# Kernel optimization log

Measured on AMD Instinct MI355X. Metric: run time of the kernel, lower is better.

## Reference

```python
import jax, jax.numpy as jnp
import numpy as np
from jax import lax

B, N, D, H, HD = 2, 2048, 2048, 16, 128
EPS = 1e-6


def setup_inputs() -> dict:
    key = jax.random.key(0)
    ks = jax.random.split(key, 6)
    x = jax.random.normal(ks[0], (B, N, D), jnp.float32)
    past_kv = jnp.zeros((B, H, HD, HD), jnp.float32)
    # positive per-head decay slopes, like MiniMax's ALiBi-style slope_rate
    slope_rate = jax.random.uniform(ks[1], (H, 1, 1), jnp.float32, 0.001, 0.1)
    w_qkv = jax.random.normal(ks[2], (3 * H * HD, D), jnp.float32) * 0.02
    w_gate = jax.random.normal(ks[3], (H * HD, D), jnp.float32) * 0.02
    w_out = jax.random.normal(ks[4], (D, H * HD), jnp.float32) * 0.02
    norm_w = jnp.ones((H * HD,), jnp.float32)
    return {"x": x, "past_kv": past_kv, "slope_rate": slope_rate,
            "w_qkv": w_qkv, "w_gate": w_gate, "w_out": w_out, "norm_w": norm_w}


def reference(x, past_kv, slope_rate, w_qkv, w_gate, w_out, norm_w):
    b, n, d = x.shape
    h = slope_rate.shape[0]
    hd = past_kv.shape[-1]

    # qkv projection + silu activation
    qkv = jax.nn.silu(x @ w_qkv.T)                 # [b, n, 3*h*hd]
    qkv = qkv.reshape(b, n, h, 3 * hd)
    q, k, v = jnp.split(qkv, 3, axis=-1)           # each [b, n, h, hd]
    # time-major for scan: [n, b, h, hd]
    q = jnp.transpose(q, (1, 0, 2, 3))
    k = jnp.transpose(k, (1, 0, 2, 3))
    v = jnp.transpose(v, (1, 0, 2, 3))

    ratio = jnp.exp(-slope_rate)                   # [h, 1, 1] broadcasts vs kv [b, h, hd, hd]

    def step(kv, qkv_t):
        q_t, k_t, v_t = qkv_t                      # each [b, h, hd]
        kv = ratio * kv + k_t[..., :, None] * v_t[..., None, :]   # [b, h, dk, dv]
        o = jnp.einsum('bhe,bhed->bhd', q_t, kv)   # contract over k-dim
        return kv, o

    kv_final, out = lax.scan(step, past_kv, (q, k, v))   # out: [n, b, h, hd]
    out = jnp.transpose(out, (1, 0, 2, 3)).reshape(b, n, h * hd)

    # RMSNorm over h*hd (computed in fp32 as in the original)
    var = jnp.mean(out * out, axis=-1, keepdims=True)
    out = norm_w * (out * lax.rsqrt(var + EPS))

    # sigmoid output gate + final projection
    gate = jax.nn.sigmoid(x @ w_gate.T)            # [b, n, h*hd]
    out = (gate * out) @ w_out.T                   # [b, n, d]
    return out, kv_final
```

## Files before the change

kernel.cpp:

```cpp
#include <hip/hip_runtime.h>


typedef __attribute__((ext_vector_type(8))) short short8;
typedef __attribute__((ext_vector_type(4))) float f32x4;

__device__ __forceinline__ float blo(unsigned int u){ return __uint_as_float(u << 16); }
__device__ __forceinline__ float bhi(unsigned int u){ return __uint_as_float(u & 0xffff0000u); }
__device__ __forceinline__ unsigned short f2b(float f){
  unsigned int u = __float_as_uint(f);
  return (unsigned short)((u + 0x7fffu + ((u >> 16) & 1u)) >> 16);
}
__device__ __forceinline__ unsigned int pk2(float a, float b){
  return (unsigned int)f2b(a) | ((unsigned int)f2b(b) << 16);
}

#define GLOAD_LDS16(g, l) __builtin_amdgcn_global_load_lds( \
    (const __attribute__((address_space(1))) unsigned int*)(g), \
    (__attribute__((address_space(3))) unsigned int*)(l), 16, 0, 0)

#define FRAG(buf, row, kt) (*(const short8*)&(buf)[(((row) << 7)) + \
    ((((((kt) << 2) + lk)) ^ ((row) & 15)) << 3)])

#define OFF_XB     ((size_t)0)
#define OFF_WQKVB  ((size_t)16777216)
#define OFF_WGATEB ((size_t)41943040)
#define OFF_WOUTB  ((size_t)50331648)
#define OFF_QB     ((size_t)58720256)
#define OFF_KB     ((size_t)75497472)
#define OFF_VTB    ((size_t)92274688)
#define OFF_KVC    ((size_t)109051904)
#define OFF_ATTN   ((size_t)142606336)
#define OFF_GATE   ((size_t)176160768)
#define OFF_YBUF   ((size_t)192937984)
#define WS_NEED    ((size_t)209715200)

__global__ __launch_bounds__(256)
void cast_f2b(const float* __restrict__ in, unsigned short* __restrict__ o, int n)
{
  int idx = (blockIdx.x * 256 + threadIdx.x) * 4;
  if (idx >= n) return;
  float4 v = *(const float4*)&in[idx];
  ushort4 u;
  u.x = f2b(v.x); u.y = f2b(v.y); u.z = f2b(v.z); u.w = f2b(v.w);
  *(ushort4*)&o[idx] = u;
}

template<int EPI>
__global__ __launch_bounds__(256)
void gemm_bt(const unsigned short* __restrict__ A, const unsigned short* __restrict__ Bm,
             int K, int Nn, void* __restrict__ o0, void* __restrict__ o1,
             void* __restrict__ o2, void* __restrict__ o3,
             const float* __restrict__ slope)
{
  __shared__ unsigned short As[4096];
  __shared__ unsigned short Bs[4096];
  const int tid  = threadIdx.x;
  const int lane = tid & 63, w = tid >> 6;
  const int mBase = blockIdx.y << 7, nBase = blockIdx.x << 7;

  f32x4 zero = {0.f, 0.f, 0.f, 0.f};
  f32x4 acc[4][4];
#pragma unroll
  for (int m = 0; m < 4; ++m)
#pragma unroll
    for (int n = 0; n < 4; ++n) acc[m][n] = zero;

  const int wr = w >> 1, wc = w & 1;
  const int rA = (wr << 6) + (lane & 15);
  const int cB = (wc << 6) + (lane & 15);
  const int kg = (lane >> 4) << 3;
  const int segBase = w << 7;
  const int nIter = K >> 5;

  for (int kt = 0; kt < nIter; ++kt) {
    const int k0 = kt << 5;
#pragma unroll
    for (int rep = 0; rep < 2; ++rep) {
      int seg = segBase + (rep << 6) + lane;
      int r  = seg >> 2;
      int c8 = (seg & 3) << 3;
      GLOAD_LDS16(A  + ((size_t)(mBase + r) * K + k0 + c8), &As[(segBase + (rep << 6)) << 3]);
      GLOAD_LDS16(Bm + ((size_t)(nBase + r) * K + k0 + c8), &Bs[(segBase + (rep << 6)) << 3]);
    }
    __syncthreads();
    short8 af[4], bfv[4];
#pragma unroll
    for (int m = 0; m < 4; ++m) af[m]  = *(const short8*)&As[((rA + (m << 4)) << 5) + kg];
#pragma unroll
    for (int n = 0; n < 4; ++n) bfv[n] = *(const short8*)&Bs[((cB + (n << 4)) << 5) + kg];
#pragma unroll
    for (int m = 0; m < 4; ++m)
#pragma unroll
      for (int n = 0; n < 4; ++n)
        acc[m][n] = __builtin_amdgcn_mfma_f32_16x16x32_bf16(af[m], bfv[n], acc[m][n], 0, 0, 0);
    __syncthreads();
  }

#pragma unroll
  for (int m = 0; m < 4; ++m) {
#pragma unroll
    for (int n = 0; n < 4; ++n) {
      const int row0 = mBase + (wr << 6) + (m << 4) + ((lane >> 4) << 2);
      const int col  = nBase + (wc << 6) + (n << 4) + (lane & 15);
      f32x4 v = acc[m][n];
#pragma unroll
      for (int i2 = 0; i2 < 4; ++i2) {
        const int row = row0 + i2;
        float val = v[i2];
        if (EPI == 0) {
          ((float*)o0)[(size_t)row * Nn + col] = val;
        } else if (EPI == 1) {
          float sv = val / (1.f + __expf(-val));
          int hh = col / 384;
          int r3 = col - hh * 384;
          int which = r3 >> 7;
          int dd = r3 & 127;
          int bb = row >> 11, nn = row & 2047;
          int bh = bb * 16 + hh;
          unsigned short sb = f2b(sv);
          size_t toff = ((size_t)bh << 18) + ((size_t)(nn >> 7) << 14)
                      + ((size_t)dd << 7) + (size_t)(nn & 127);
          if (which == 0) {
            ((unsigned short*)o0)[(((size_t)bh << 11) + nn) * 128 + dd] = sb;
          } else if (which == 1) {
            ((unsigned short*)o1)[(((size_t)bh << 11) + nn) * 128 + dd] = sb;
            float lam = __expf(-slope[hh] * (float)(127 - (nn & 127)));
            ((unsigned short*)o3)[toff] = f2b(sv * lam);
          } else {
            ((unsigned short*)o2)[toff] = sb;
          }
        } else {
          float sg = 1.f / (1.f + __expf(-val));
          ((unsigned short*)o0)[(size_t)row * Nn + col] = f2b(sg);
        }
      }
    }
  }
}

__global__ __launch_bounds__(256, 2)
void chunk_kv_mfma(const unsigned short* __restrict__ vtg,
                   const unsigned short* __restrict__ ktg,
                   float* __restrict__ KVc)
{
  __shared__ unsigned short VTs[16384], KTs[16384];
  const int blk = blockIdx.x;
  const int tid = threadIdx.x, lane = tid & 63, w = tid >> 6;
  const int wr = w >> 1, wc = w & 1, lr = lane & 15, lk = lane >> 4;
  const size_t base = (size_t)blk << 14;
#pragma unroll
  for (int it = 0; it < 8; ++it) {
    int segw = (w << 3) + it;
    int sg = (segw << 6) + lane;
    int r = sg >> 4, sl = sg & 15;
    size_t goff = ((size_t)r << 7) + (size_t)((sl ^ (r & 15)) << 3);
    GLOAD_LDS16(vtg + base + goff, &VTs[segw << 9]);
    GLOAD_LDS16(ktg + base + goff, &KTs[segw << 9]);
  }
  __syncthreads();
  f32x4 zero = {0.f,0.f,0.f,0.f};
  f32x4 acc[4][4];
#pragma unroll
  for (int m = 0; m < 4; ++m)
#pragma unroll
    for (int n = 0; n < 4; ++n) acc[m][n] = zero;
#pragma unroll
  for (int kt = 0; kt < 4; ++kt) {
    short8 af[4], bf2[4];
#pragma unroll
    for (int m = 0; m < 4; ++m) af[m]  = FRAG(VTs, (wr << 6) + (m << 4) + lr, kt);
#pragma unroll
    for (int n = 0; n < 4; ++n) bf2[n] = FRAG(KTs, (wc << 6) + (n << 4) + lr, kt);
#pragma unroll
    for (int m = 0; m < 4; ++m)
#pragma unroll
      for (int n = 0; n < 4; ++n)
        acc[m][n] = __builtin_amdgcn_mfma_f32_16x16x32_bf16(af[m], bf2[n], acc[m][n], 0, 0, 0);
  }
  float* outp = KVc + base;
#pragma unroll
  for (int m = 0; m < 4; ++m)
#pragma unroll
    for (int n = 0; n < 4; ++n)
#pragma unroll
      for (int r2 = 0; r2 < 4; ++r2)
        outp[(size_t)((wr << 6) + (m << 4) + (lk << 2) + r2) * 128
             + (wc << 6) + (n << 4) + lr] = acc[m][n][r2];
}

__global__ __launch_bounds__(256)
void combine_kv(float* __restrict__ KVc, const float* __restrict__ past_kv,
                const float* __restrict__ slope, float* __restrict__ outkv)
{
  const int bh = blockIdx.x >> 3, slice = blockIdx.x & 7;
  const int h = bh & 15;
  const int tid = threadIdx.x;
  const float lamC = __expf(-slope[h] * 128.f);
  const int f0 = (slice << 11) + tid;
  float S[8];
  const float* pp = past_kv + ((size_t)bh << 14);
#pragma unroll
  for (int i = 0; i < 8; ++i) {
    int f = f0 + (i << 8);
    int d = f >> 7, e = f & 127;
    S[i] = pp[(e << 7) + d];
  }
  for (int cc = 0; cc < 16; ++cc) {
    float* p = KVc + ((((size_t)bh << 4) + cc) << 14);
#pragma unroll
    for (int i = 0; i < 8; ++i) {
      int f = f0 + (i << 8);
      float t = p[f];
      p[f] = S[i];
      S[i] = lamC * S[i] + t;
    }
  }
  float* op = outkv + ((size_t)bh << 14);
#pragma unroll
  for (int i = 0; i < 8; ++i) {
    int f = f0 + (i << 8);
    int d = f >> 7, e = f & 127;
    op[(e << 7) + d] = S[i];
  }
}

__global__ __launch_bounds__(256, 1)
void chunk_out_mfma(const unsigned short* __restrict__ qg,
                    const unsigned short* __restrict__ kg,
                    const unsigned short* __restrict__ vtg,
                    const float* __restrict__ States,
                    const float* __restrict__ slope,
                    float* __restrict__ attn)
{
  __shared__ unsigned short Qs[16384], Ks[16384], VTs[16384], STs[16384];
  const int blk = blockIdx.x;
  const int cc = blk & 15, h = (blk >> 4) & 15, b = blk >> 8;
  const int tid = threadIdx.x, lane = tid & 63, w = tid >> 6;
  const int wr = w >> 1, wc = w & 1, lr = lane & 15, lk = lane >> 4;
  const size_t base = (size_t)blk << 14;
  const float s = slope[h];

#pragma unroll
  for (int it = 0; it < 8; ++it) {
    int segw = (w << 3) + it;
    int sg = (segw << 6) + lane;
    int r = sg >> 4, sl = sg & 15;
    size_t goff = ((size_t)r << 7) + (size_t)((sl ^ (r & 15)) << 3);
    GLOAD_LDS16(qg  + base + goff, &Qs[segw << 9]);
    GLOAD_LDS16(kg  + base + goff, &Ks[segw << 9]);
    GLOAD_LDS16(vtg + base + goff, &VTs[segw << 9]);
  }
  const float* Sg = States + base;
#pragma unroll
  for (int it = 0; it < 8; ++it) {
    int idx = ((it << 8) + tid) << 3;
    float4 a0 = *(const float4*)&Sg[idx];
    float4 a1 = *(const float4*)&Sg[idx + 4];
    int r = idx >> 7, c = idx & 127;
    int sl = (c >> 3) ^ (r & 15);
    uint4 u = make_uint4(pk2(a0.x,a0.y), pk2(a0.z,a0.w), pk2(a1.x,a1.y), pk2(a1.z,a1.w));
    *(uint4*)&STs[(r << 7) + (sl << 3)] = u;
  }
  __syncthreads();

  f32x4 zero = {0.f,0.f,0.f,0.f};
  f32x4 Oa[4][4], Pa[4][4];
#pragma unroll
  for (int m = 0; m < 4; ++m)
#pragma unroll
    for (int n = 0; n < 4; ++n) { Oa[m][n] = zero; Pa[m][n] = zero; }

#pragma unroll
  for (int kt = 0; kt < 4; ++kt) {
    short8 qf[4], bst[4], bk[4];
#pragma unroll
    for (int m = 0; m < 4; ++m) qf[m] = FRAG(Qs, (wr << 6) + (m << 4) + lr, kt);
#pragma unroll
    for (int n = 0; n < 4; ++n) {
      int cn = (wc << 6) + (n << 4) + lr;
      bst[n] = FRAG(STs, cn, kt);
      bk[n]  = FRAG(Ks,  cn, kt);
    }
#pragma unroll
    for (int m = 0; m < 4; ++m)
#pragma unroll
      for (int n = 0; n < 4; ++n) {
        Oa[m][n] = __builtin_amdgcn_mfma_f32_16x16x32_bf16(qf[m], bst[n], Oa[m][n], 0, 0, 0);
        Pa[m][n] = __builtin_amdgcn_mfma_f32_16x16x32_bf16(qf[m], bk[n],  Pa[m][n], 0, 0, 0);
      }
  }

  float emi[16];
#pragma unroll
  for (int m = 0; m < 4; ++m)
#pragma unroll
    for (int r2 = 0; r2 < 4; ++r2)
      emi[(m << 2) + r2] = __expf(-s * (float)((wr << 6) + (m << 4) + (lk << 2) + r2));
  const float lam1 = __expf(-s);
  float epj[4];
#pragma unroll
  for (int n = 0; n < 4; ++n)
    epj[n] = __expf(s * (float)((wc << 6) + (n << 4) + lr));

#pragma unroll
  for (int m = 0; m < 4; ++m)
#pragma unroll
    for (int n = 0; n < 4; ++n) {
      const int j = (wc << 6) + (n << 4) + lr;
#pragma unroll
      for (int r2 = 0; r2 < 4; ++r2) {
        const int i = (wr << 6) + (m << 4) + (lk << 2) + r2;
        Oa[m][n][r2] *= emi[(m << 2) + r2] * lam1;
        float pv = Pa[m][n][r2] * emi[(m << 2) + r2] * epj[n];
        Pa[m][n][r2] = (i >= j) ? pv : 0.f;
      }
    }
  __syncthreads();

#pragma unroll
  for (int m = 0; m < 4; ++m)
#pragma unroll
    for (int n = 0; n < 4; ++n) {
      const int j = (wc << 6) + (n << 4) + lr;
#pragma unroll
      for (int r2 = 0; r2 < 4; ++r2) {
        const int i = (wr << 6) + (m << 4) + (lk << 2) + r2;
        const int sl = (j >> 3) ^ (i & 15);
        Ks[(i << 7) + (sl << 3) + (j & 7)] = f2b(Pa[m][n][r2]);
      }
    }
  __syncthreads();

#pragma unroll
  for (int kt = 0; kt < 4; ++kt) {
    short8 pf[4], vf[4];
#pragma unroll
    for (int m = 0; m < 4; ++m) pf[m] = FRAG(Ks,  (wr << 6) + (m << 4) + lr, kt);
#pragma unroll
    for (int n = 0; n < 4; ++n) vf[n] = FRAG(VTs, (wc << 6) + (n << 4) + lr, kt);
#pragma unroll
    for (int m = 0; m < 4; ++m)
#pragma unroll
      for (int n = 0; n < 4; ++n)
        Oa[m][n] = __builtin_amdgcn_mfma_f32_16x16x32_bf16(pf[m], vf[n], Oa[m][n], 0, 0, 0);
  }

#pragma unroll
  for (int m = 0; m < 4; ++m)
#pragma unroll
    for (int n = 0; n < 4; ++n) {
      const int c = (wc << 6) + (n << 4) + lr;
#pragma unroll
      for (int r2 = 0; r2 < 4; ++r2) {
        const int i = (wr << 6) + (m << 4) + (lk << 2) + r2;
        attn[(((size_t)((b << 11) + (cc << 7) + i)) << 11) + (h << 7) + c] = Oa[m][n][r2];
      }
    }
}

__global__ __launch_bounds__(256)
void norm_gate(const float* __restrict__ attn, const unsigned short* __restrict__ gateb,
               const float* __restrict__ normw, unsigned short* __restrict__ ybuf)
{
  const int row = blockIdx.x;
  const int tid = threadIdx.x;
  const float* ar = attn + ((size_t)row << 11);
  float4 v0 = *(const float4*)&ar[tid * 8];
  float4 v1 = *(const float4*)&ar[tid * 8 + 4];
  float ss = v0.x*v0.x + v0.y*v0.y + v0.z*v0.z + v0.w*v0.w
           + v1.x*v1.x + v1.y*v1.y + v1.z*v1.z + v1.w*v1.w;
#pragma unroll
  for (int off = 32; off > 0; off >>= 1) ss += __shfl_down(ss, off);
  __shared__ float red[4];
  if ((tid & 63) == 0) red[tid >> 6] = ss;
  __syncthreads();
  float tot = red[0] + red[1] + red[2] + red[3];
  float scale = rsqrtf(tot * (1.f / 2048.f) + 1e-6f);
  uint4 gg = *(const uint4*)&gateb[((size_t)row << 11) + tid * 8];
  float4 w0 = *(const float4*)&normw[tid * 8];
  float4 w1 = *(const float4*)&normw[tid * 8 + 4];
  ushort4 o0, o1;
  o0.x = f2b(v0.x * scale * w0.x * blo(gg.x));
  o0.y = f2b(v0.y * scale * w0.y * bhi(gg.x));
  o0.z = f2b(v0.z * scale * w0.z * blo(gg.y));
  o0.w = f2b(v0.w * scale * w0.w * bhi(gg.y));
  o1.x = f2b(v1.x * scale * w1.x * blo(gg.z));
  o1.y = f2b(v1.y * scale * w1.y * bhi(gg.z));
  o1.z = f2b(v1.z * scale * w1.z * blo(gg.w));
  o1.w = f2b(v1.w * scale * w1.w * bhi(gg.w));
  *(ushort4*)&ybuf[((size_t)row << 11) + tid * 8]     = o0;
  *(ushort4*)&ybuf[((size_t)row << 11) + tid * 8 + 4] = o1;
}

extern "C" void kernel_launch(void* const* d_in, const int* in_sizes, int n_in,
                              void* d_out, int out_size, void* d_ws, size_t ws_size,
                              hipStream_t stream)
{
  const float* x       = (const float*)d_in[0];
  const float* past_kv = (const float*)d_in[1];
  const float* slope   = (const float*)d_in[2];
  const float* w_qkv   = (const float*)d_in[3];
  const float* w_gate  = (const float*)d_in[4];
  const float* w_out   = (const float*)d_in[5];
  const float* norm_w  = (const float*)d_in[6];
  float* out    = (float*)d_out;
  float* out_kv = out + 8388608;
  if (ws_size < WS_NEED) return;
  char* ws = (char*)d_ws;
  unsigned short* xb     = (unsigned short*)(ws + OFF_XB);
  unsigned short* wqkvb  = (unsigned short*)(ws + OFF_WQKVB);
  unsigned short* wgateb = (unsigned short*)(ws + OFF_WGATEB);
  unsigned short* woutb  = (unsigned short*)(ws + OFF_WOUTB);
  unsigned short* qb     = (unsigned short*)(ws + OFF_QB);
  unsigned short* kb     = (unsigned short*)(ws + OFF_KB);
  unsigned short* vtb    = (unsigned short*)(ws + OFF_VTB);
  unsigned short* ktb    = (unsigned short*)(ws + OFF_YBUF);
  float*          kvc    = (float*)(ws + OFF_KVC);
  float*          attn   = (float*)(ws + OFF_ATTN);
  unsigned short* gate   = (unsigned short*)(ws + OFF_GATE);
  unsigned short* ybuf   = (unsigned short*)(ws + OFF_YBUF);

  cast_f2b<<<8192,  256, 0, stream>>>(x,      xb,     8388608);
  cast_f2b<<<12288, 256, 0, stream>>>(w_qkv,  wqkvb,  12582912);
  cast_f2b<<<4096,  256, 0, stream>>>(w_gate, wgateb, 4194304);
  cast_f2b<<<4096,  256, 0, stream>>>(w_out,  woutb,  4194304);

  gemm_bt<1><<<dim3(48, 32), 256, 0, stream>>>(xb, wqkvb, 2048, 6144,
                                               qb, kb, vtb, ktb, slope);
  gemm_bt<2><<<dim3(16, 32), 256, 0, stream>>>(xb, wgateb, 2048, 2048,
                                               gate, nullptr, nullptr, nullptr, nullptr);

  chunk_kv_mfma<<<512, 256, 0, stream>>>(vtb, ktb, kvc);
  combine_kv   <<<256, 256, 0, stream>>>(kvc, past_kv, slope, out_kv);
  chunk_out_mfma<<<512, 256, 0, stream>>>(qb, kb, vtb, kvc, slope, attn);

  norm_gate<<<4096, 256, 0, stream>>>(attn, gate, norm_w, ybuf);
  gemm_bt<0><<<dim3(16, 32), 256, 0, stream>>>(ybuf, woutb, 2048, 2048,
                                               out, nullptr, nullptr, nullptr, nullptr);
}
```

Measured before the change: 519.4 us.

## Fuse gate GEMM into QKV GEMM and stage transposed K/V stores through LDS

The separate sigmoid-gate GEMM is folded into the QKV GEMM launch by widening the output to 8192 columns. This assumes the bf16 gate weights sit directly after the QKV weights in the workspace. The epilogue is restructured per block: q/k are written row-wise, while the transposed v and decay-scaled k tiles are first staged through a swizzled LDS buffer and then written with 16-byte coalesced stores. The aim is to remove the strided 2-byte scattered stores and one kernel launch, at the cost of a larger LDS footprint and an extra barrier in the epilogue.

```diff
diff --git a/kernel.cpp b/kernel.cpp
--- a/kernel.cpp
+++ b/kernel.cpp
@@ -49,11 +49,12 @@
 __global__ __launch_bounds__(256)
 void gemm_bt(const unsigned short* __restrict__ A, const unsigned short* __restrict__ Bm,
              int K, int Nn, void* __restrict__ o0, void* __restrict__ o1,
-             void* __restrict__ o2, void* __restrict__ o3,
+             void* __restrict__ o2, void* __restrict__ o3, void* __restrict__ o4,
              const float* __restrict__ slope)
 {
-  __shared__ unsigned short As[4096];
-  __shared__ unsigned short Bs[4096];
+  __shared__ unsigned short S[(EPI == 1) ? 16384 : 8192];
+  unsigned short* Asp = S;
+  unsigned short* Bsp = S + 4096;
   const int tid  = threadIdx.x;
   const int lane = tid & 63, w = tid >> 6;
   const int mBase = blockIdx.y << 7, nBase = blockIdx.x << 7;
@@ -79,15 +80,15 @@
       int seg = segBase + (rep << 6) + lane;
       int r  = seg >> 2;
       int c8 = (seg & 3) << 3;
-      GLOAD_LDS16(A  + ((size_t)(mBase + r) * K + k0 + c8), &As[(segBase + (rep << 6)) << 3]);
-      GLOAD_LDS16(Bm + ((size_t)(nBase + r) * K + k0 + c8), &Bs[(segBase + (rep << 6)) << 3]);
+      GLOAD_LDS16(A  + ((size_t)(mBase + r) * K + k0 + c8), &Asp[(segBase + (rep << 6)) << 3]);
+      GLOAD_LDS16(Bm + ((size_t)(nBase + r) * K + k0 + c8), &Bsp[(segBase + (rep << 6)) << 3]);
     }
     __syncthreads();
     short8 af[4], bfv[4];
 #pragma unroll
-    for (int m = 0; m < 4; ++m) af[m]  = *(const short8*)&As[((rA + (m << 4)) << 5) + kg];
-#pragma unroll
-    for (int n = 0; n < 4; ++n) bfv[n] = *(const short8*)&Bs[((cB + (n << 4)) << 5) + kg];
+    for (int m = 0; m < 4; ++m) af[m]  = *(const short8*)&Asp[((rA + (m << 4)) << 5) + kg];
+#pragma unroll
+    for (int n = 0; n < 4; ++n) bfv[n] = *(const short8*)&Bsp[((cB + (n << 4)) << 5) + kg];
 #pragma unroll
     for (int m = 0; m < 4; ++m)
 #pragma unroll
@@ -96,42 +97,88 @@
     __syncthreads();
   }
 
-#pragma unroll
-  for (int m = 0; m < 4; ++m) {
-#pragma unroll
-    for (int n = 0; n < 4; ++n) {
-      const int row0 = mBase + (wr << 6) + (m << 4) + ((lane >> 4) << 2);
-      const int col  = nBase + (wc << 6) + (n << 4) + (lane & 15);
-      f32x4 v = acc[m][n];
-#pragma unroll
-      for (int i2 = 0; i2 < 4; ++i2) {
-        const int row = row0 + i2;
-        float val = v[i2];
-        if (EPI == 0) {
-          ((float*)o0)[(size_t)row * Nn + col] = val;
-        } else if (EPI == 1) {
-          float sv = val / (1.f + __expf(-val));
-          int hh = col / 384;
-          int r3 = col - hh * 384;
-          int which = r3 >> 7;
-          int dd = r3 & 127;
-          int bb = row >> 11, nn = row & 2047;
-          int bh = bb * 16 + hh;
-          unsigned short sb = f2b(sv);
-          size_t toff = ((size_t)bh << 18) + ((size_t)(nn >> 7) << 14)
-                      + ((size_t)dd << 7) + (size_t)(nn & 127);
-          if (which == 0) {
-            ((unsigned short*)o0)[(((size_t)bh << 11) + nn) * 128 + dd] = sb;
-          } else if (which == 1) {
-            ((unsigned short*)o1)[(((size_t)bh << 11) + nn) * 128 + dd] = sb;
-            float lam = __expf(-slope[hh] * (float)(127 - (nn & 127)));
-            ((unsigned short*)o3)[toff] = f2b(sv * lam);
-          } else {
-            ((unsigned short*)o2)[toff] = sb;
+  const int lk4 = (lane >> 4) << 2;
+  if (EPI == 0) {
+#pragma unroll
+    for (int m = 0; m < 4; ++m)
+#pragma unroll
+      for (int n = 0; n < 4; ++n) {
+        const int row0 = mBase + (wr << 6) + (m << 4) + lk4;
+        const int col  = nBase + (wc << 6) + (n << 4) + (lane & 15);
+        f32x4 v = acc[m][n];
+#pragma unroll
+        for (int r2 = 0; r2 < 4; ++r2)
+          ((float*)o0)[(size_t)(row0 + r2) * Nn + col] = v[r2];
+      }
+  } else {
+    const int bb = mBase >> 11, cc = (mBase & 2047) >> 7;
+    int which, hh = 0;
+    if (nBase >= 6144) { which = 3; }
+    else { hh = nBase / 384; which = (nBase - hh * 384) >> 7; }
+    const int bh = (bb << 4) + hh;
+
+#pragma unroll
+    for (int m = 0; m < 4; ++m) {
+#pragma unroll
+      for (int n = 0; n < 4; ++n) {
+        const int lrow = (wr << 6) + (m << 4) + lk4;
+        const int dloc = (wc << 6) + (n << 4) + (lane & 15);
+        f32x4 v = acc[m][n];
+        if (which == 3) {
+#pragma unroll
+          for (int r2 = 0; r2 < 4; ++r2) {
+            float sg = 1.f / (1.f + __expf(-v[r2]));
+            ((unsigned short*)o4)[((size_t)(mBase + lrow + r2) << 11)
+                                  + (nBase - 6144) + dloc] = f2b(sg);
           }
         } else {
-          float sg = 1.f / (1.f + __expf(-val));
-          ((unsigned short*)o0)[(size_t)row * Nn + col] = f2b(sg);
+          float sv[4];
+#pragma unroll
+          for (int r2 = 0; r2 < 4; ++r2) sv[r2] = v[r2] / (1.f + __expf(-v[r2]));
+          if (which <= 1) {
+            unsigned short* dst = (which == 0) ? (unsigned short*)o0 : (unsigned short*)o1;
+#pragma unroll
+            for (int r2 = 0; r2 < 4; ++r2) {
+              int nn = (mBase & 2047) + lrow + r2;
+              dst[(((size_t)bh << 11) + nn) * 128 + dloc] = f2b(sv[r2]);
+            }
+          }
+          if (which >= 1) {
+            int sidx = (dloc << 7) + ((((lrow >> 2) ^ (dloc & 31))) << 2);
+            *(unsigned int*)&S[sidx]     = pk2(sv[0], sv[1]);
+            *(unsigned int*)&S[sidx + 2] = pk2(sv[2], sv[3]);
+          }
+        }
+      }
+    }
+    if (which == 1 || which == 2) {
+      __syncthreads();
+      const int nnc = tid & 15, dd0 = (tid >> 4) << 3;
+      const int nn0 = nnc << 3;
+      const size_t baseT = ((size_t)((bh << 4) + cc) << 14);
+      float lamf[8];
+      if (which == 1) {
+        const float s = slope[hh];
+#pragma unroll
+        for (int t = 0; t < 8; ++t) lamf[t] = __expf(-s * (float)(127 - (nn0 + t)));
+      }
+#pragma unroll
+      for (int i = 0; i < 8; ++i) {
+        const int dd = dd0 + i;
+        const int s0 = (((nnc << 1)     ) ^ (dd & 31)) << 2;
+        const int s1 = (((nnc << 1) | 1 ) ^ (dd & 31)) << 2;
+        uint2 a  = *(const uint2*)&S[(dd << 7) + s0];
+        uint2 b2 = *(const uint2*)&S[(dd << 7) + s1];
+        if (which == 1) {
+          a.x  = pk2(blo(a.x)  * lamf[0], bhi(a.x)  * lamf[1]);
+          a.y  = pk2(blo(a.y)  * lamf[2], bhi(a.y)  * lamf[3]);
+          b2.x = pk2(blo(b2.x) * lamf[4], bhi(b2.x) * lamf[5]);
+          b2.y = pk2(blo(b2.y) * lamf[6], bhi(b2.y) * lamf[7]);
+          *(uint4*)((unsigned short*)o3 + baseT + ((size_t)dd << 7) + nn0)
+              = make_uint4(a.x, a.y, b2.x, b2.y);
+        } else {
+          *(uint4*)((unsigned short*)o2 + baseT + ((size_t)dd << 7) + nn0)
+              = make_uint4(a.x, a.y, b2.x, b2.y);
         }
       }
     }
@@ -425,10 +472,8 @@
   cast_f2b<<<4096,  256, 0, stream>>>(w_gate, wgateb, 4194304);
   cast_f2b<<<4096,  256, 0, stream>>>(w_out,  woutb,  4194304);
 
-  gemm_bt<1><<<dim3(48, 32), 256, 0, stream>>>(xb, wqkvb, 2048, 6144,
-                                               qb, kb, vtb, ktb, slope);
-  gemm_bt<2><<<dim3(16, 32), 256, 0, stream>>>(xb, wgateb, 2048, 2048,
-                                               gate, nullptr, nullptr, nullptr, nullptr);
+  gemm_bt<1><<<dim3(64, 32), 256, 0, stream>>>(xb, wqkvb, 2048, 8192,
+                                               qb, kb, vtb, ktb, gate, slope);
 
   chunk_kv_mfma<<<512, 256, 0, stream>>>(vtb, ktb, kvc);
   combine_kv   <<<256, 256, 0, stream>>>(kvc, past_kv, slope, out_kv);
@@ -436,5 +481,5 @@
 
   norm_gate<<<4096, 256, 0, stream>>>(attn, gate, norm_w, ybuf);
   gemm_bt<0><<<dim3(16, 32), 256, 0, stream>>>(ybuf, woutb, 2048, 2048,
-                                               out, nullptr, nullptr, nullptr, nullptr);
-}
+                                               out, nullptr, nullptr, nullptr, nullptr, nullptr);
+}
```

New measurement: 472.3 us. -9.1%, faster.

## Fuse QKV and gate GEMMs into pipelined 256x256 tile kernel, split transposes out

Applied to the files above, without the earlier changes.

Replaces the two separate 128x128 projection GEMMs with one 512-thread kernel over the concatenated QKV and gate weights. It uses 256x256 tiles, double-buffered LDS staging interleaved with MFMA phases, s_setprio, and a grouped block swizzle. The scattered transposed K/V writes move out of the GEMM epilogue into a new LDS-based transpose kernel (tkv), which also applies the decay scaling to K. This adds a kernel launch and an extra round trip of K/V through memory in exchange for a denser, coalesced, overlapped main GEMM.

```diff
diff --git a/kernel.cpp b/kernel.cpp
--- a/kernel.cpp
+++ b/kernel.cpp
@@ -45,33 +45,203 @@
   *(ushort4*)&o[idx] = u;
 }
 
-template<int EPI>
+__global__ __launch_bounds__(512, 2)
+void gemm256_qkvg(const unsigned short* __restrict__ A, const unsigned short* __restrict__ Bm,
+                  const float* __restrict__ slope,
+                  unsigned short* __restrict__ qo, unsigned short* __restrict__ ko,
+                  unsigned short* __restrict__ vo, unsigned short* __restrict__ go)
+{
+  __shared__ unsigned short lds[65536];
+  const int tid = threadIdx.x, lane = tid & 63, w = tid >> 6;
+  const int wm = w >> 2, wn = w & 3;
+  const int lr = lane & 15, kg = lane >> 4;
+
+  const int bid = blockIdx.x;
+  const int swz = ((bid & 7) << 6) + (bid >> 3);
+  const int mBase = (swz >> 5) << 8;
+  const int nBase = (swz & 31) << 8;
+
+  auto stage = [&](const unsigned short* __restrict__ src, int rowBase, int k0,
+                   unsigned short* lb, int half) {
+#pragma unroll
+    for (int s = 0; s < 2; ++s) {
+      const int idx = (s << 9) + tid;
+      const int r = idx >> 3, sl = idx & 7;
+      GLOAD_LDS16(src + (size_t)(rowBase + (half << 7) + r) * 2048 + k0
+                      + ((sl ^ (r & 7)) << 3),
+                  lb + (half << 13) + (((s << 9) + (w << 6)) << 3));
+    }
+  };
+
+  f32x4 acc[8][4];
+#pragma unroll
+  for (int m = 0; m < 8; ++m)
+#pragma unroll
+    for (int n = 0; n < 4; ++n) acc[m][n] = (f32x4){0.f, 0.f, 0.f, 0.f};
+
+  const int NT = 32;
+  stage(A,  mBase, 0, lds,        0);
+  stage(A,  mBase, 0, lds,        1);
+  stage(Bm, nBase, 0, lds + 16384, 0);
+  stage(Bm, nBase, 0, lds + 16384, 1);
+  __syncthreads();
+
+  for (int t = 0; t < NT; ++t) {
+    unsigned short* Ab = lds + ((t & 1) << 15);
+    unsigned short* Bb = Ab + 16384;
+    unsigned short* An = lds + (((t & 1) ^ 1) << 15);
+    unsigned short* Bn = An + 16384;
+    const int k0n = (t + 1) << 6;
+#pragma unroll
+    for (int p = 0; p < 4; ++p) {
+      if (t + 1 < NT) {
+        if      (p == 0) stage(A,  mBase, k0n, An, 0);
+        else if (p == 1) stage(A,  mBase, k0n, An, 1);
+        else if (p == 2) stage(Bm, nBase, k0n, Bn, 0);
+        else             stage(Bm, nBase, k0n, Bn, 1);
+      }
+      const int mh = p >> 1, nh = p & 1;
+      short8 af[4][2], bf[2][2];
+#pragma unroll
+      for (int m = 0; m < 4; ++m) {
+        const int rA = (wm << 7) + (mh << 6) + (m << 4) + lr;
+#pragma unroll
+        for (int ks = 0; ks < 2; ++ks)
+          af[m][ks] = *(const short8*)&Ab[(rA << 6) + ((((ks << 2) + kg) ^ (rA & 7)) << 3)];
+      }
+#pragma unroll
+      for (int n = 0; n < 2; ++n) {
+        const int rB = (wn << 6) + (nh << 5) + (n << 4) + lr;
+#pragma unroll
+        for (int ks = 0; ks < 2; ++ks)
+          bf[n][ks] = *(const short8*)&Bb[(rB << 6) + ((((ks << 2) + kg) ^ (rB & 7)) << 3)];
+      }
+      __builtin_amdgcn_s_setprio(1);
+#pragma unroll
+      for (int m = 0; m < 4; ++m)
+#pragma unroll
+        for (int n = 0; n < 2; ++n)
+#pragma unroll
+          for (int ks = 0; ks < 2; ++ks)
+            acc[(mh << 2) + m][(nh << 1) + n] =
+              __builtin_amdgcn_mfma_f32_16x16x32_bf16(af[m][ks], bf[n][ks],
+                  acc[(mh << 2) + m][(nh << 1) + n], 0, 0, 0);
+      __builtin_amdgcn_s_setprio(0);
+      if (p < 3) __builtin_amdgcn_s_barrier();
+    }
+    __syncthreads();
+  }
+
+  const int cb = nBase + (wn << 6);
+  const int rowW = mBase + (wm << 7);
+  if (cb >= 6144) {
+#pragma unroll
+    for (int mi = 0; mi < 8; ++mi)
+#pragma unroll
+      for (int ni = 0; ni < 4; ++ni) {
+        f32x4 v = acc[mi][ni];
+        const int colg = cb - 6144 + (ni << 4) + lr;
+#pragma unroll
+        for (int r2 = 0; r2 < 4; ++r2) {
+          const int row = rowW + (mi << 4) + (kg << 2) + r2;
+          go[((size_t)row << 11) + colg] = f2b(1.f / (1.f + __expf(-v[r2])));
+        }
+      }
+  } else {
+    const int hh = cb / 384;
+    const int rem = cb - hh * 384;
+    const int sub = rem >> 7;
+    const int db = rem & 127;
+    unsigned short* dst = (sub == 0) ? qo : (sub == 1) ? ko : vo;
+#pragma unroll
+    for (int mi = 0; mi < 8; ++mi)
+#pragma unroll
+      for (int ni = 0; ni < 4; ++ni) {
+        f32x4 v = acc[mi][ni];
+        const int dd = db + (ni << 4) + lr;
+#pragma unroll
+        for (int r2 = 0; r2 < 4; ++r2) {
+          const int row = rowW + (mi << 4) + (kg << 2) + r2;
+          const int bb = row >> 11, nn = row & 2047;
+          float sv = v[r2] / (1.f + __expf(-v[r2]));
+          dst[(((size_t)((bb << 4) + hh) << 11) + nn) * 128 + dd] = f2b(sv);
+        }
+      }
+  }
+}
+
 __global__ __launch_bounds__(256)
-void gemm_bt(const unsigned short* __restrict__ A, const unsigned short* __restrict__ Bm,
-             int K, int Nn, void* __restrict__ o0, void* __restrict__ o1,
-             void* __restrict__ o2, void* __restrict__ o3,
-             const float* __restrict__ slope)
+void tkv(const unsigned short* __restrict__ kg_, const unsigned short* __restrict__ vg_,
+         const float* __restrict__ slope, unsigned short* __restrict__ kto,
+         unsigned short* __restrict__ vto)
+{
+  __shared__ unsigned int T[8192];
+  __shared__ float lamt[128];
+  const int blk = blockIdx.x;
+  const int h = (blk >> 4) & 15;
+  const int tid = threadIdx.x;
+  const size_t base = (size_t)blk << 14;
+  if (tid < 128) lamt[tid] = __expf(-slope[h] * (float)(127 - tid));
+#pragma unroll
+  for (int pass = 0; pass < 2; ++pass) {
+    const unsigned short* src = pass ? vg_ : kg_;
+    __syncthreads();
+#pragma unroll
+    for (int it = 0; it < 4; ++it) {
+      const int j = ((tid >> 4) << 1) + (it << 5);
+      const int d0 = (tid & 15) << 3;
+      uint4 a  = *(const uint4*)&src[base + (size_t)j * 128 + d0];
+      uint4 b2 = *(const uint4*)&src[base + (size_t)(j + 1) * 128 + d0];
+      const unsigned short* ap = (const unsigned short*)&a;
+      const unsigned short* bp = (const unsigned short*)&b2;
+      const int jp = j >> 1;
+#pragma unroll
+      for (int t2 = 0; t2 < 8; ++t2) {
+        const int d = d0 + t2;
+        T[(d << 6) + (jp ^ (((d >> 3) & 15) << 2))] =
+            (unsigned int)ap[t2] | ((unsigned int)bp[t2] << 16);
+      }
+    }
+    __syncthreads();
+#pragma unroll
+    for (int it = 0; it < 8; ++it) {
+      const int d = (tid >> 4) + (it << 4);
+      const int jp0 = (tid & 15) << 2;
+      uint4 u = *(const uint4*)&T[(d << 6) + (jp0 ^ (((d >> 3) & 15) << 2))];
+      const int j0 = jp0 << 1;
+      if (pass == 0) {
+        u.x = pk2(blo(u.x) * lamt[j0],     bhi(u.x) * lamt[j0 + 1]);
+        u.y = pk2(blo(u.y) * lamt[j0 + 2], bhi(u.y) * lamt[j0 + 3]);
+        u.z = pk2(blo(u.z) * lamt[j0 + 4], bhi(u.z) * lamt[j0 + 5]);
+        u.w = pk2(blo(u.w) * lamt[j0 + 6], bhi(u.w) * lamt[j0 + 7]);
+        *(uint4*)&kto[base + ((size_t)d << 7) + j0] = u;
+      } else {
+        *(uint4*)&vto[base + ((size_t)d << 7) + j0] = u;
+      }
+    }
+  }
+}
+
+__global__ __launch_bounds__(256)
+void gemm_out(const unsigned short* __restrict__ A, const unsigned short* __restrict__ Bm,
+              int K, int Nn, float* __restrict__ o0)
 {
   __shared__ unsigned short As[4096];
   __shared__ unsigned short Bs[4096];
   const int tid  = threadIdx.x;
   const int lane = tid & 63, w = tid >> 6;
   const int mBase = blockIdx.y << 7, nBase = blockIdx.x << 7;
-
-  f32x4 zero = {0.f, 0.f, 0.f, 0.f};
   f32x4 acc[4][4];
 #pragma unroll
   for (int m = 0; m < 4; ++m)
 #pragma unroll
-    for (int n = 0; n < 4; ++n) acc[m][n] = zero;
-
+    for (int n = 0; n < 4; ++n) acc[m][n] = (f32x4){0.f,0.f,0.f,0.f};
   const int wr = w >> 1, wc = w & 1;
   const int rA = (wr << 6) + (lane & 15);
   const int cB = (wc << 6) + (lane & 15);
   const int kg = (lane >> 4) << 3;
   const int segBase = w << 7;
   const int nIter = K >> 5;
-
   for (int kt = 0; kt < nIter; ++kt) {
     const int k0 = kt << 5;
 #pragma unroll
@@ -95,47 +265,17 @@
         acc[m][n] = __builtin_amdgcn_mfma_f32_16x16x32_bf16(af[m], bfv[n], acc[m][n], 0, 0, 0);
     __syncthreads();
   }
-
-#pragma unroll
-  for (int m = 0; m < 4; ++m) {
+#pragma unroll
+  for (int m = 0; m < 4; ++m)
 #pragma unroll
     for (int n = 0; n < 4; ++n) {
       const int row0 = mBase + (wr << 6) + (m << 4) + ((lane >> 4) << 2);
       const int col  = nBase + (wc << 6) + (n << 4) + (lane & 15);
       f32x4 v = acc[m][n];
 #pragma unroll
-      for (int i2 = 0; i2 < 4; ++i2) {
-        const int row = row0 + i2;
-        float val = v[i2];
-        if (EPI == 0) {
-          ((float*)o0)[(size_t)row * Nn + col] = val;
-        } else if (EPI == 1) {
-          float sv = val / (1.f + __expf(-val));
-          int hh = col / 384;
-          int r3 = col - hh * 384;
-          int which = r3 >> 7;
-          int dd = r3 & 127;
-          int bb = row >> 11, nn = row & 2047;
-          int bh = bb * 16 + hh;
-          unsigned short sb = f2b(sv);
-          size_t toff = ((size_t)bh << 18) + ((size_t)(nn >> 7) << 14)
-                      + ((size_t)dd << 7) + (size_t)(nn & 127);
-          if (which == 0) {
-            ((unsigned short*)o0)[(((size_t)bh << 11) + nn) * 128 + dd] = sb;
-          } else if (which == 1) {
-            ((unsigned short*)o1)[(((size_t)bh << 11) + nn) * 128 + dd] = sb;
-            float lam = __expf(-slope[hh] * (float)(127 - (nn & 127)));
-            ((unsigned short*)o3)[toff] = f2b(sv * lam);
-          } else {
-            ((unsigned short*)o2)[toff] = sb;
-          }
-        } else {
-          float sg = 1.f / (1.f + __expf(-val));
-          ((unsigned short*)o0)[(size_t)row * Nn + col] = f2b(sg);
-        }
-      }
-    }
-  }
+      for (int r2 = 0; r2 < 4; ++r2)
+        o0[(size_t)(row0 + r2) * Nn + col] = v[r2];
+    }
 }
 
 __global__ __launch_bounds__(256, 2)
@@ -158,12 +298,11 @@
     GLOAD_LDS16(ktg + base + goff, &KTs[segw << 9]);
   }
   __syncthreads();
-  f32x4 zero = {0.f,0.f,0.f,0.f};
   f32x4 acc[4][4];
 #pragma unroll
   for (int m = 0; m < 4; ++m)
 #pragma unroll
-    for (int n = 0; n < 4; ++n) acc[m][n] = zero;
+    for (int n = 0; n < 4; ++n) acc[m][n] = (f32x4){0.f,0.f,0.f,0.f};
 #pragma unroll
   for (int kt = 0; kt < 4; ++kt) {
     short8 af[4], bf2[4];
@@ -239,7 +378,6 @@
   const int wr = w >> 1, wc = w & 1, lr = lane & 15, lk = lane >> 4;
   const size_t base = (size_t)blk << 14;
   const float s = slope[h];
-
 #pragma unroll
   for (int it = 0; it < 8; ++it) {
     int segw = (w << 3) + it;
@@ -263,12 +401,11 @@
   }
   __syncthreads();
 
-  f32x4 zero = {0.f,0.f,0.f,0.f};
   f32x4 Oa[4][4], Pa[4][4];
 #pragma unroll
   for (int m = 0; m < 4; ++m)
 #pragma unroll
-    for (int n = 0; n < 4; ++n) { Oa[m][n] = zero; Pa[m][n] = zero; }
+    for (int n = 0; n < 4; ++n) { Oa[m][n] = (f32x4){0.f,0.f,0.f,0.f}; Pa[m][n] = (f32x4){0.f,0.f,0.f,0.f}; }
 
 #pragma unroll
   for (int kt = 0; kt < 4; ++kt) {
@@ -414,6 +551,7 @@
   unsigned short* qb     = (unsigned short*)(ws + OFF_QB);
   unsigned short* kb     = (unsigned short*)(ws + OFF_KB);
   unsigned short* vtb    = (unsigned short*)(ws + OFF_VTB);
+  unsigned short* vrow   = (unsigned short*)(ws + OFF_ATTN);
   unsigned short* ktb    = (unsigned short*)(ws + OFF_YBUF);
   float*          kvc    = (float*)(ws + OFF_KVC);
   float*          attn   = (float*)(ws + OFF_ATTN);
@@ -425,16 +563,14 @@
   cast_f2b<<<4096,  256, 0, stream>>>(w_gate, wgateb, 4194304);
   cast_f2b<<<4096,  256, 0, stream>>>(w_out,  woutb,  4194304);
 
-  gemm_bt<1><<<dim3(48, 32), 256, 0, stream>>>(xb, wqkvb, 2048, 6144,
-                                               qb, kb, vtb, ktb, slope);
-  gemm_bt<2><<<dim3(16, 32), 256, 0, stream>>>(xb, wgateb, 2048, 2048,
-                                               gate, nullptr, nullptr, nullptr, nullptr);
-
-  chunk_kv_mfma<<<512, 256, 0, stream>>>(vtb, ktb, kvc);
-  combine_kv   <<<256, 256, 0, stream>>>(kvc, past_kv, slope, out_kv);
+  gemm256_qkvg<<<512, 512, 0, stream>>>(xb, wqkvb, slope, qb, kb, vrow, gate);
+
+  tkv<<<512, 256, 0, stream>>>(kb, vrow, slope, ktb, vtb);
+
+  chunk_kv_mfma <<<512, 256, 0, stream>>>(vtb, ktb, kvc);
+  combine_kv    <<<256, 256, 0, stream>>>(kvc, past_kv, slope, out_kv);
   chunk_out_mfma<<<512, 256, 0, stream>>>(qb, kb, vtb, kvc, slope, attn);
 
   norm_gate<<<4096, 256, 0, stream>>>(attn, gate, norm_w, ybuf);
-  gemm_bt<0><<<dim3(16, 32), 256, 0, stream>>>(ybuf, woutb, 2048, 2048,
-                                               out, nullptr, nullptr, nullptr, nullptr);
-}
+  gemm_out<<<dim3(16, 32), 256, 0, stream>>>(ybuf, woutb, 2048, 2048, out);
+}
```

New measurement: 429.1 us. 17.4% less time.
